# Optimization experiments

Measured on AMD Instinct MI355X. Metric: run time of the kernel, lower is better.

Reference implementation:

```python
import jax, jax.numpy as jnp
import numpy as np


def setup_inputs() -> dict:
    key = jax.random.key(0)
    k1, k2 = jax.random.split(key)
    B, S, D, K = 16, 2048, 256, 512
    features = jax.random.normal(k1, (B, S, D), dtype=jnp.float32)
    Ck = jax.random.normal(k2, (1, K, D), dtype=jnp.float32)
    return {"features": features, "Ck": Ck}


def reference(features, Ck):
    # features: (B, S, D); Ck: (1, K, D)
    # Squared euclidean distance to each of K centers: (B, S, K)
    # Computed as ||f||^2 + ||c||^2 - 2 f.c to avoid the (B*S, K, D) diff tensor.
    C = Ck[0]                                   # (K, D)
    f_sq = jnp.sum(features * features, axis=-1, keepdims=True)   # (B, S, 1)
    c_sq = jnp.sum(C * C, axis=-1)                                # (K,)
    cross = jnp.einsum("bsd,kd->bsk", features, C)               # (B, S, K)
    return f_sq + c_sq[None, None, :] - 2.0 * cross
```

## Files before the change

### kernel.cpp

```cpp
#include <hip/hip_runtime.h>

typedef __attribute__((ext_vector_type(8))) short bf16x8;
typedef __attribute__((ext_vector_type(4))) float f32x4;

#define D_DIM 256
#define BM 128
#define BN 128
#define BK 128

__device__ inline unsigned short f2bf(float f) {
  unsigned int u = __builtin_bit_cast(unsigned int, f);
  u += 0x7fffu + ((u >> 16) & 1u);
  return (unsigned short)(u >> 16);
}

__device__ inline void gload16(const void* g, void* l) {
  __builtin_amdgcn_global_load_lds(
      (const __attribute__((address_space(1))) void*)g,
      (__attribute__((address_space(3))) void*)l, 16, 0, 0);
}

__global__ void prep_rows(const float* __restrict__ F, const float* __restrict__ C,
                          unsigned short* __restrict__ Abf, unsigned short* __restrict__ Cbf,
                          float* __restrict__ fsq, float* __restrict__ csq, int M) {
  const int w = threadIdx.x >> 6, lane = threadIdx.x & 63;
  int row = blockIdx.x * 4 + w;
  const float* src;
  unsigned short* dst;
  float* rsq;
  if (row < M) {
    src = F; dst = Abf; rsq = fsq;
  } else {
    row -= M;
    src = C; dst = Cbf; rsq = csq;
  }
  const float4 v = *reinterpret_cast<const float4*>(&src[(size_t)row * D_DIM + lane * 4]);
  ushort4 b;
  b.x = f2bf(v.x); b.y = f2bf(v.y); b.z = f2bf(v.z); b.w = f2bf(v.w);
  const int boff = (lane * 8) ^ ((row & 7) << 4);
  *reinterpret_cast<ushort4*>((char*)dst + (size_t)row * 512 + boff) = b;
  float sq = v.x * v.x + v.y * v.y + v.z * v.z + v.w * v.w;
#pragma unroll
  for (int o = 32; o; o >>= 1) sq += __shfl_xor(sq, o);
  if (lane == 0) rsq[row] = sq;
}

__global__ __launch_bounds__(256, 2) void dist_gemm(
    const unsigned short* __restrict__ A, const unsigned short* __restrict__ B,
    const float* __restrict__ fsq, const float* __restrict__ csq,
    float* __restrict__ out, int M, int N) {
  __shared__ unsigned short As[BM * BK];
  __shared__ unsigned short Bs[BN * BK];

  const int t = threadIdx.x;
  const int w = t >> 6, lane = t & 63;
  const int wr = w >> 1, wc = w & 1;
  const int rl = lane & 15, kh = lane >> 4;

  const int nwg = gridDim.x;
  const int cpx = nwg >> 3;
  const int work = (blockIdx.x & 7) * cpx + (blockIdx.x >> 3);
  const int ntiles = N / BN;
  const int n0 = (work % ntiles) * BN;
  const int m0 = (work / ntiles) * BM;

  float fr[4][4];
#pragma unroll
  for (int mi = 0; mi < 4; mi++)
#pragma unroll
    for (int r = 0; r < 4; r++)
      fr[mi][r] = fsq[m0 + wr * 64 + mi * 16 + kh * 4 + r];
  float cs[4];
#pragma unroll
  for (int ni = 0; ni < 4; ni++)
    cs[ni] = csq[n0 + wc * 64 + ni * 16 + rl];

  f32x4 acc[4][4];
#pragma unroll
  for (int i = 0; i < 4; i++)
#pragma unroll
    for (int j = 0; j < 4; j++) acc[i][j] = (f32x4){0.f, 0.f, 0.f, 0.f};

  const int srow = t >> 4;
  const int scb = (t & 15) * 16;

  for (int kt = 0; kt < 2; ++kt) {
    const size_t ktoff = (size_t)kt * 256;
#pragma unroll
    for (int j = 0; j < 8; ++j) {
      const int row = j * 16 + srow;
      gload16((const char*)A + (size_t)(m0 + row) * 512 + ktoff + scb,
              (char*)As + j * 4096 + w * 1024);
      gload16((const char*)B + (size_t)(n0 + row) * 512 + ktoff + scb,
              (char*)Bs + j * 4096 + w * 1024);
    }
    __syncthreads();
#pragma unroll
    for (int kk = 0; kk < 4; ++kk) {
      const int doff = kk * 64 + kh * 16;
      const int soff = doff ^ ((rl & 7) << 4);
      bf16x8 af[4], bfr[4];
#pragma unroll
      for (int mi = 0; mi < 4; mi++)
        af[mi] = *reinterpret_cast<const bf16x8*>(
            (const char*)As + (wr * 64 + mi * 16 + rl) * 256 + soff);
#pragma unroll
      for (int ni = 0; ni < 4; ni++)
        bfr[ni] = *reinterpret_cast<const bf16x8*>(
            (const char*)Bs + (wc * 64 + ni * 16 + rl) * 256 + soff);
#pragma unroll
      for (int mi = 0; mi < 4; mi++)
#pragma unroll
        for (int ni = 0; ni < 4; ni++)
          acc[mi][ni] = __builtin_amdgcn_mfma_f32_16x16x32_bf16(
              af[mi], bfr[ni], acc[mi][ni], 0, 0, 0);
    }
    __syncthreads();
  }

#pragma unroll
  for (int mi = 0; mi < 4; mi++) {
    const int rloc = wr * 64 + mi * 16 + kh * 4;
#pragma unroll
    for (int ni = 0; ni < 4; ni++) {
      const int cloc = wc * 64 + ni * 16 + rl;
#pragma unroll
      for (int r = 0; r < 4; r++)
        out[(size_t)(m0 + rloc + r) * N + n0 + cloc] =
            fr[mi][r] + cs[ni] - 2.0f * acc[mi][ni][r];
    }
  }
}

extern "C" void kernel_launch(void* const* d_in, const int* in_sizes, int n_in,
                              void* d_out, int out_size, void* d_ws, size_t ws_size,
                              hipStream_t stream) {
  const float* F = (const float*)d_in[0];
  const float* C = (const float*)d_in[1];
  float* out = (float*)d_out;
  const int M = in_sizes[0] / D_DIM;
  const int N = in_sizes[1] / D_DIM;

  unsigned short* Abf = (unsigned short*)d_ws;
  unsigned short* Cbf = Abf + (size_t)M * D_DIM;
  float* fsq = (float*)(Cbf + (size_t)N * D_DIM);
  float* csq = fsq + M;

  hipLaunchKernelGGL(prep_rows, dim3((M + N) / 4), dim3(256), 0, stream,
                     F, C, Abf, Cbf, fsq, csq, M);
  const int nwg = (M / BM) * (N / BN);
  hipLaunchKernelGGL(dist_gemm, dim3(nwg), dim3(256), 0, stream,
                     Abf, Cbf, fsq, csq, out, M, N);
}
```

Before: 32.74 us.

## Double-buffer LDS K tiles with BK=64 to overlap global loads and MFMA

Halves the K tile to 64 and adds two LDS buffers. The loads for the next K slice are issued before computing on the current one, with explicit vmcnt waits and raw s_barrier calls replacing __syncthreads. LDS usage stays the same (2x16KB per matrix), so occupancy is unchanged. The intent is to hide global-to-LDS latency behind MFMA work, at the cost of more barriers and a prologue load.

```diff
diff --git a/kernel.cpp b/kernel.cpp
--- a/kernel.cpp
+++ b/kernel.cpp
@@ -6,7 +6,7 @@
 #define D_DIM 256
 #define BM 128
 #define BN 128
-#define BK 128
+#define BK 64
 
 __device__ inline unsigned short f2bf(float f) {
   unsigned int u = __builtin_bit_cast(unsigned int, f);
@@ -49,13 +49,14 @@
     const unsigned short* __restrict__ A, const unsigned short* __restrict__ B,
     const float* __restrict__ fsq, const float* __restrict__ csq,
     float* __restrict__ out, int M, int N) {
-  __shared__ unsigned short As[BM * BK];
-  __shared__ unsigned short Bs[BN * BK];
+  __shared__ __align__(16) char As[2][BM * 128];
+  __shared__ __align__(16) char Bs[2][BN * 128];
 
   const int t = threadIdx.x;
   const int w = t >> 6, lane = t & 63;
   const int wr = w >> 1, wc = w & 1;
   const int rl = lane & 15, kh = lane >> 4;
+  const int amask = (rl & 7) << 4;
 
   const int nwg = gridDim.x;
   const int cpx = nwg >> 3;
@@ -63,6 +64,18 @@
   const int ntiles = N / BN;
   const int n0 = (work % ntiles) * BN;
   const int m0 = (work / ntiles) * BM;
+
+  const int s_row = t >> 3;
+  const int s_cb = (t & 7) * 16;
+  const char* Asrc = (const char*)A + (size_t)(m0 + s_row) * 512 + s_cb;
+  const char* Bsrc = (const char*)B + (size_t)(n0 + s_row) * 512 + s_cb;
+
+#pragma unroll
+  for (int j = 0; j < 4; ++j)
+    gload16(Asrc + j * 16384, (char*)As[0] + j * 4096 + w * 1024);
+#pragma unroll
+  for (int j = 0; j < 4; ++j)
+    gload16(Bsrc + j * 16384, (char*)Bs[0] + j * 4096 + w * 1024);
 
   float fr[4][4];
 #pragma unroll
@@ -81,33 +94,36 @@
 #pragma unroll
     for (int j = 0; j < 4; j++) acc[i][j] = (f32x4){0.f, 0.f, 0.f, 0.f};
 
-  const int srow = t >> 4;
-  const int scb = (t & 15) * 16;
+#pragma unroll
+  for (int kt = 0; kt < 4; ++kt) {
+    const int cur = kt & 1;
+    if (kt < 3) {
+      const int nxt = cur ^ 1;
+#pragma unroll
+      for (int j = 0; j < 4; ++j)
+        gload16(Asrc + (kt + 1) * 128 + j * 16384, (char*)As[nxt] + j * 4096 + w * 1024);
+#pragma unroll
+      for (int j = 0; j < 4; ++j)
+        gload16(Bsrc + (kt + 1) * 128 + j * 16384, (char*)Bs[nxt] + j * 4096 + w * 1024);
+      asm volatile("s_waitcnt vmcnt(8)" ::: "memory");
+    } else {
+      asm volatile("s_waitcnt vmcnt(0)" ::: "memory");
+    }
+    __builtin_amdgcn_s_barrier();
+    asm volatile("" ::: "memory");
 
-  for (int kt = 0; kt < 2; ++kt) {
-    const size_t ktoff = (size_t)kt * 256;
 #pragma unroll
-    for (int j = 0; j < 8; ++j) {
-      const int row = j * 16 + srow;
-      gload16((const char*)A + (size_t)(m0 + row) * 512 + ktoff + scb,
-              (char*)As + j * 4096 + w * 1024);
-      gload16((const char*)B + (size_t)(n0 + row) * 512 + ktoff + scb,
-              (char*)Bs + j * 4096 + w * 1024);
-    }
-    __syncthreads();
-#pragma unroll
-    for (int kk = 0; kk < 4; ++kk) {
-      const int doff = kk * 64 + kh * 16;
-      const int soff = doff ^ ((rl & 7) << 4);
+    for (int kk = 0; kk < 2; ++kk) {
+      const int soff = (kk * 64 + kh * 16) ^ amask;
       bf16x8 af[4], bfr[4];
 #pragma unroll
       for (int mi = 0; mi < 4; mi++)
         af[mi] = *reinterpret_cast<const bf16x8*>(
-            (const char*)As + (wr * 64 + mi * 16 + rl) * 256 + soff);
+            (const char*)As[cur] + (wr * 64 + mi * 16 + rl) * 128 + soff);
 #pragma unroll
       for (int ni = 0; ni < 4; ni++)
         bfr[ni] = *reinterpret_cast<const bf16x8*>(
-            (const char*)Bs + (wc * 64 + ni * 16 + rl) * 256 + soff);
+            (const char*)Bs[cur] + (wc * 64 + ni * 16 + rl) * 128 + soff);
 #pragma unroll
       for (int mi = 0; mi < 4; mi++)
 #pragma unroll
@@ -115,7 +131,8 @@
           acc[mi][ni] = __builtin_amdgcn_mfma_f32_16x16x32_bf16(
               af[mi], bfr[ni], acc[mi][ni], 0, 0, 0);
     }
-    __syncthreads();
+    __builtin_amdgcn_s_barrier();
+    asm volatile("" ::: "memory");
   }
 
 #pragma unroll
```

New measurement: 32.39 us. About the same (-1.0%).
